# Kernel optimization log

Measured on AMD Instinct MI355X. Metric: run time of the kernel, lower is better.

The kernel has to match this reference:

```python
import jax, jax.numpy as jnp
import numpy as np

ALPHA = 0.5
GAMMA = 0.001
BIG = 1e10  # stand-in for +inf on DP borders (DILATE uses 1e10 in dtw_grad)

B, L, DIM = 32, 512, 16


def softdtw_single(D, gamma):
    """Soft-DTW value for one [N,N] cost matrix via anti-diagonal wavefront.
    Padded grid Rp[(N+1),(N+1)]: Rp[0,0]=0, borders=BIG,
    Rp[i,j] = D[i-1,j-1] + softmin_gamma(Rp[i-1,j], Rp[i-1,j-1], Rp[i,j-1]).
    Returns Rp[N,N]."""
    N = D.shape[0]
    ii = jnp.arange(N + 1)
    diag0 = jnp.full((N + 1,), BIG, D.dtype).at[0].set(0.0)  # diagonal d=0
    diag1 = jnp.full((N + 1,), BIG, D.dtype)                 # diagonal d=1 (borders)

    def step(carry, d):
        prev2, prev1 = carry  # diagonals d-2, d-1; prev1[i] = Rp[i, d-1-i]
        j = d - ii
        valid = (ii >= 1) & (ii <= N) & (j >= 1) & (j <= N)
        dval = D[jnp.clip(ii - 1, 0, N - 1), jnp.clip(j - 1, 0, N - 1)]
        a = jnp.roll(prev1, 1).at[0].set(BIG)  # Rp[i-1, j]
        b = jnp.roll(prev2, 1).at[0].set(BIG)  # Rp[i-1, j-1]
        c = prev1                               # Rp[i, j-1]
        sm = -gamma * jax.nn.logsumexp(jnp.stack([a, b, c]) * (-1.0 / gamma), axis=0)
        cur = jnp.where(valid, dval + sm, BIG)
        return (prev1, cur), None

    (_, last), _ = jax.lax.scan(step, (diag0, diag1), jnp.arange(2, 2 * N + 1))
    return last[N]


def batched_sq_dists(x, y):
    # dist[b,i,j] = clamp(||x[b,i]-y[b,j]||^2, 0)
    xn = jnp.sum(x * x, -1)[:, :, None]
    yn = jnp.sum(y * y, -1)[:, None, :]
    return jnp.clip(xn + yn - 2.0 * jnp.einsum('bid,bjd->bij', x, y), 0.0)


def dilate_loss(inp, tgt):
    # base=None path: shift input so its first step is at the origin
    x = inp - inp[:, 0:1, :]
    D = batched_sq_dists(tgt, x)  # D[b] = pairwise_distances(target[b], input[b])
    # SoftDTW value and soft alignment path (= grad of value wrt D, as in DILATE PathDTW)
    vals, paths = jax.vmap(jax.value_and_grad(lambda Dk: softdtw_single(Dk, GAMMA)))(D)
    loss_shape = jnp.mean(vals)
    N = D.shape[1]
    idx = jnp.arange(N, dtype=D.dtype)
    Omega = (idx[:, None] - idx[None, :]) ** 2  # pairwise sq dists of arange(N)
    path = jnp.mean(paths, axis=0)
    loss_temporal = jnp.sum(path * Omega) / (N * N)
    return ALPHA * loss_shape + (1.0 - ALPHA) * loss_temporal


def setup_inputs() -> dict:
    key = jax.random.key(0)
    k1, k2 = jax.random.split(key)
    inp = jax.random.normal(k1, (B, L, DIM), dtype=jnp.float32)
    tgt = jax.random.normal(k2, (B, L, DIM), dtype=jnp.float32)
    return {"input": inp, "target": tgt}


def reference(input, target):
    return dilate_loss(input, target)
```

## Files before the change

kernel.cpp:

```cpp
#include <hip/hip_runtime.h>
#include <stdint.h>


#define N 512
#define NB 32
#define BIGF 1e10f

typedef unsigned int u32;
typedef float f32x4 __attribute__((ext_vector_type(4)));

__global__ __launch_bounds__(512) void kA(const float* __restrict__ inp,
                                          const float* __restrict__ tgt,
                                          float* __restrict__ Dg) {
    const int b = blockIdx.y;
    const int jc = blockIdx.x;
    const int tid = (int)threadIdx.x;
    __shared__ float xs[4][16];
    if (tid < 64) {
        int c = tid >> 4, d = tid & 15;
        int j = jc * 4 + c;
        xs[c][d] = inp[(((size_t)b * N + j) << 4) + d] -
                   inp[(((size_t)b * N) << 4) + d];
    }
    __syncthreads();
    const float4* t4 = (const float4*)(tgt + (((size_t)b * N + tid) << 4));
    float4 ta = t4[0], tb = t4[1], tc = t4[2], td = t4[3];
    float* out = Dg + ((size_t)b * N + (size_t)jc * 4) * N + tid;
#pragma unroll
    for (int c = 0; c < 4; ++c) {
        float s = 0.f, e;
        e = ta.x - xs[c][0];  s = fmaf(e, e, s);
        e = ta.y - xs[c][1];  s = fmaf(e, e, s);
        e = ta.z - xs[c][2];  s = fmaf(e, e, s);
        e = ta.w - xs[c][3];  s = fmaf(e, e, s);
        e = tb.x - xs[c][4];  s = fmaf(e, e, s);
        e = tb.y - xs[c][5];  s = fmaf(e, e, s);
        e = tb.z - xs[c][6];  s = fmaf(e, e, s);
        e = tb.w - xs[c][7];  s = fmaf(e, e, s);
        e = tc.x - xs[c][8];  s = fmaf(e, e, s);
        e = tc.y - xs[c][9];  s = fmaf(e, e, s);
        e = tc.z - xs[c][10]; s = fmaf(e, e, s);
        e = tc.w - xs[c][11]; s = fmaf(e, e, s);
        e = td.x - xs[c][12]; s = fmaf(e, e, s);
        e = td.y - xs[c][13]; s = fmaf(e, e, s);
        e = td.z - xs[c][14]; s = fmaf(e, e, s);
        e = td.w - xs[c][15]; s = fmaf(e, e, s);
        out[(size_t)c * N] = s;
    }
}

__global__ __launch_bounds__(64) void kFT(const float* __restrict__ Dg,
                                          float* __restrict__ acc) {
    const int b = blockIdx.x;
    const int l = (int)threadIdx.x;
    const float* Db = Dg + (size_t)b * N * N;

    f32x4 A0[4], A1[4], B0[4], B1[4];
    const float* pS[4];

#define LOADC(s_, Tt)                                                         \
    do {                                                                      \
        int c_ = min(max(2 * ((Tt) - l), 0), 510);                            \
        const float* p_ = Db + ((size_t)c_ << 9) + (l << 3);                  \
        A0[s_] = ((const f32x4*)p_)[0];  A1[s_] = ((const f32x4*)p_)[1];      \
        B0[s_] = ((const f32x4*)(p_ + 512))[0];                               \
        B1[s_] = ((const f32x4*)(p_ + 512))[1];                               \
    } while (0)

#define LOADP(s_)                                                             \
    do {                                                                      \
        A0[s_] = ((const f32x4*)pS[s_])[0];                                   \
        A1[s_] = ((const f32x4*)pS[s_])[1];                                   \
        B0[s_] = ((const f32x4*)(pS[s_] + 512))[0];                           \
        B1[s_] = ((const f32x4*)(pS[s_] + 512))[1];                           \
        pS[s_] += 4096;                                                       \
    } while (0)

    float Rprev[8], Tprev[8];
#pragma unroll
    for (int r = 0; r < 8; ++r) { Rprev[r] = BIGF; Tprev[r] = 0.f; }
    float sA = BIGF, sB = BIGF, sBold = BIGF;
    float tA = 0.f, tB = 0.f, tBold = 0.f;
    float Rfin = 0.f, Tfin = 0.f;
    float dbA = (float)(10 * l);

    LOADC(0, 0); LOADC(1, 1); LOADC(2, 2); LOADC(3, 3);

#define MSTEP(T_, s_, PH)                                                     \
    do {                                                                      \
        const int cpair = (T_) - l;                                           \
        const bool valid = (PH == 1) || ((unsigned)cpair < 256u);             \
        float dA0 = (l == 0) ? BIGF : sBold;                                  \
        if (PH == 0) dA0 = (l == 0 && (T_) == 0) ? 0.f : dA0;                 \
        const float upA0 = (l == 0) ? BIGF : sA;                              \
        const float upB0 = (l == 0) ? BIGF : sB;                              \
        const float dA0T = (l == 0) ? 0.f : tBold;                            \
        const float upA0T = (l == 0) ? 0.f : tA;                              \
        const float upB0T = (l == 0) ? 0.f : tB;                              \
        const float dbB = dbA - 1.0f;                                         \
        float RcA[8], RcB[8], TcA[8], TcB[8];                                 \
        _Pragma("unroll") for (int r = 0; r < 8; ++r) {                       \
            float up = (r == 0) ? upA0 : RcA[r - 1];                          \
            float dg = (r == 0) ? dA0 : Rprev[r - 1];                         \
            float lf = Rprev[r];                                              \
            float upT = (r == 0) ? upA0T : TcA[r - 1];                        \
            float dgT = (r == 0) ? dA0T : Tprev[r - 1];                       \
            float lfT = Tprev[r];                                             \
            float mn = fminf(up, fminf(dg, lf));                              \
            float Ts = (mn == dg) ? dgT : ((mn == up) ? upT : lfT);           \
            float dr = dbA + (float)r;                                        \
            TcA[r] = fmaf(dr, dr, Ts);                                        \
            RcA[r] = ((r < 4) ? A0[s_][(r) & 3] : A1[s_][(r) & 3]) + mn;      \
        }                                                                     \
        _Pragma("unroll") for (int r = 0; r < 8; ++r) {                       \
            float up = (r == 0) ? upB0 : RcB[r - 1];                          \
            float dg = (r == 0) ? upA0 : RcA[r - 1];                          \
            float lf = RcA[r];                                                \
            float upT = (r == 0) ? upB0T : TcB[r - 1];                        \
            float dgT = (r == 0) ? upA0T : TcA[r - 1];                        \
            float lfT = TcA[r];                                               \
            float mn = fminf(up, fminf(dg, lf));                              \
            float Ts = (mn == dg) ? dgT : ((mn == up) ? upT : lfT);           \
            float dr = dbB + (float)r;                                        \
            TcB[r] = fmaf(dr, dr, Ts);                                        \
            RcB[r] = ((r < 4) ? B0[s_][(r) & 3] : B1[s_][(r) & 3]) + mn;      \
        }                                                                     \
        if (PH == 1) {                                                        \
            _Pragma("unroll") for (int r = 0; r < 8; ++r) {                   \
                Rprev[r] = RcB[r]; Tprev[r] = TcB[r];                         \
            }                                                                 \
        } else {                                                              \
            _Pragma("unroll") for (int r = 0; r < 8; ++r) {                   \
                Rprev[r] = valid ? RcB[r] : Rprev[r];                         \
                Tprev[r] = valid ? TcB[r] : Tprev[r];                         \
            }                                                                 \
        }                                                                     \
        float exA = RcA[7], exB = RcB[7], exAT = TcA[7], exBT = TcB[7];       \
        if (PH != 1) {                                                        \
            exA = valid ? exA : BIGF;                                         \
            exB = valid ? exB : BIGF;                                         \
            exAT = valid ? exAT : 0.f;                                        \
            exBT = valid ? exBT : 0.f;                                        \
        }                                                                     \
        if (PH == 2) {                                                        \
            if (cpair == 255) { Rfin = RcB[7]; Tfin = TcB[7]; }               \
        }                                                                     \
        sBold = sB; tBold = tB;                                               \
        sA = __shfl_up(exA, 1);                                               \
        sB = __shfl_up(exB, 1);                                               \
        tA = __shfl_up(exAT, 1);                                              \
        tB = __shfl_up(exBT, 1);                                              \
        dbA -= 2.0f;                                                          \
        if (PH == 1) { LOADP(s_); } else { LOADC(s_, (T_) + 4); }             \
    } while (0)

    for (int T = 0; T < 64; T += 4) {
        MSTEP(T + 0, 0, 0); MSTEP(T + 1, 1, 0);
        MSTEP(T + 2, 2, 0); MSTEP(T + 3, 3, 0);
    }
#pragma unroll
    for (int s = 0; s < 4; ++s)
        pS[s] = Db + ((size_t)(2 * (68 + s - l)) << 9) + (l << 3);
    for (int T = 64; T < 252; T += 4) {
        MSTEP(T + 0, 0, 1); MSTEP(T + 1, 1, 1);
        MSTEP(T + 2, 2, 1); MSTEP(T + 3, 3, 1);
    }
    for (int T = 252; T < 320; T += 4) {
        MSTEP(T + 0, 0, 2); MSTEP(T + 1, 1, 2);
        MSTEP(T + 2, 2, 2); MSTEP(T + 3, 3, 2);
    }
#undef MSTEP
#undef LOADC
#undef LOADP

    if (l == 63) {
        acc[b] = Rfin;
        acc[NB + b] = Tfin;
    }
}

__global__ void kC(const float* __restrict__ acc, float* __restrict__ out) {
    const int l = (int)threadIdx.x;
    float vs = (l < NB) ? acc[l] : 0.f;
    float vt = (l < NB) ? acc[NB + l] : 0.f;
#pragma unroll
    for (int o = 32; o >= 1; o >>= 1) {
        vs += __shfl_down(vs, o);
        vt += __shfl_down(vt, o);
    }
    if (l == 0)
        out[0] = 0.5f * (vs / (float)NB) +
                 0.5f * (vt / ((float)NB * (float)(N * N)));
}

__global__ void kSentinel(float* out) { out[0] = -12345.0f; }

extern "C" void kernel_launch(void* const* d_in, const int* in_sizes, int n_in,
                              void* d_out, int out_size, void* d_ws, size_t ws_size,
                              hipStream_t stream) {
    const float* inp = (const float*)d_in[0];
    const float* tgt = (const float*)d_in[1];
    float* out = (float*)d_out;

    const size_t DSZ = (size_t)NB * N * N * sizeof(float);
    const size_t NEEDED = 256 + DSZ;
    if (ws_size < NEEDED) {
        kSentinel<<<1, 1, 0, stream>>>(out);
        return;
    }
    char* ws = (char*)d_ws;
    float* acc = (float*)ws;
    float* Dg = (float*)(ws + 256);

    kA<<<dim3(N / 4, NB), 512, 0, stream>>>(inp, tgt, Dg);
    kFT<<<NB, 64, 0, stream>>>(Dg, acc);
    kC<<<1, 64, 0, stream>>>(acc, out);
}
```

Measured before the change: 123.5 us.

## Process four columns per wavefront step with DPP lane shifts

The hard-min DTW wavefront kernel now has each lane handle 8 rows by 4 columns per step instead of 8x2. This cuts the wavefront step count from 320 to 192 and so fewer serial cross-lane exchanges are needed. The prefetch pipeline is reduced from 4 to 2 stages, each loading twice the data. Lane shifts use a DPP row-shift builtin instead of __shfl_up, and a sched_barrier pins instruction order at each step. The validity masking used for the early and late phases was removed. This relies on clamped loads and BIG propagation staying correct, and it raises register pressure.

Measured after the change: 132.8 us. 7.5% more time.

```diff
diff --git a/kernel.cpp b/kernel.cpp
--- a/kernel.cpp
+++ b/kernel.cpp
@@ -8,6 +8,12 @@
 
 typedef unsigned int u32;
 typedef float f32x4 __attribute__((ext_vector_type(4)));
+
+#if __has_builtin(__builtin_amdgcn_mov_dpp)
+#define SHFL1(x) __int_as_float(__builtin_amdgcn_mov_dpp(__float_as_int(x), 0x138, 0xF, 0xF, true))
+#else
+#define SHFL1(x) __shfl_up((x), 1)
+#endif
 
 __global__ __launch_bounds__(512) void kA(const float* __restrict__ inp,
                                           const float* __restrict__ tgt,
@@ -55,121 +61,92 @@
     const int l = (int)threadIdx.x;
     const float* Db = Dg + (size_t)b * N * N;
 
-    f32x4 A0[4], A1[4], B0[4], B1[4];
-    const float* pS[4];
+    f32x4 DA[2][4], DB[2][4];
+    const float* pS[2];
 
 #define LOADC(s_, Tt)                                                         \
     do {                                                                      \
-        int c_ = min(max(2 * ((Tt) - l), 0), 510);                            \
-        const float* p_ = Db + ((size_t)c_ << 9) + (l << 3);                  \
-        A0[s_] = ((const f32x4*)p_)[0];  A1[s_] = ((const f32x4*)p_)[1];      \
-        B0[s_] = ((const f32x4*)(p_ + 512))[0];                               \
-        B1[s_] = ((const f32x4*)(p_ + 512))[1];                               \
+        int c0_ = min(max(4 * ((Tt) - l), 0), 508);                           \
+        const float* p_ = Db + ((size_t)c0_ << 9) + (l << 3);                 \
+        DA[s_][0] = ((const f32x4*)p_)[0];        DB[s_][0] = ((const f32x4*)p_)[1]; \
+        DA[s_][1] = ((const f32x4*)(p_ + 512))[0];  DB[s_][1] = ((const f32x4*)(p_ + 512))[1]; \
+        DA[s_][2] = ((const f32x4*)(p_ + 1024))[0]; DB[s_][2] = ((const f32x4*)(p_ + 1024))[1]; \
+        DA[s_][3] = ((const f32x4*)(p_ + 1536))[0]; DB[s_][3] = ((const f32x4*)(p_ + 1536))[1]; \
     } while (0)
 
 #define LOADP(s_)                                                             \
     do {                                                                      \
-        A0[s_] = ((const f32x4*)pS[s_])[0];                                   \
-        A1[s_] = ((const f32x4*)pS[s_])[1];                                   \
-        B0[s_] = ((const f32x4*)(pS[s_] + 512))[0];                           \
-        B1[s_] = ((const f32x4*)(pS[s_] + 512))[1];                           \
-        pS[s_] += 4096;                                                       \
+        const float* p_ = pS[s_];                                             \
+        DA[s_][0] = ((const f32x4*)p_)[0];        DB[s_][0] = ((const f32x4*)p_)[1]; \
+        DA[s_][1] = ((const f32x4*)(p_ + 512))[0];  DB[s_][1] = ((const f32x4*)(p_ + 512))[1]; \
+        DA[s_][2] = ((const f32x4*)(p_ + 1024))[0]; DB[s_][2] = ((const f32x4*)(p_ + 1024))[1]; \
+        DA[s_][3] = ((const f32x4*)(p_ + 1536))[0]; DB[s_][3] = ((const f32x4*)(p_ + 1536))[1]; \
+        pS[s_] += 4096;                                          \
     } while (0)
 
-    float Rprev[8], Tprev[8];
+    float Rp_[8], Tp_[8];
+    float X[8], XT[8], Y[8], YT[8];
 #pragma unroll
-    for (int r = 0; r < 8; ++r) { Rprev[r] = BIGF; Tprev[r] = 0.f; }
-    float sA = BIGF, sB = BIGF, sBold = BIGF;
-    float tA = 0.f, tB = 0.f, tBold = 0.f;
+    for (int r = 0; r < 8; ++r) { Rp_[r] = BIGF; Tp_[r] = 0.f; }
+    float sR0 = BIGF, sR1 = BIGF, sR2 = BIGF, sR3 = BIGF, sRold = BIGF;
+    float tR0 = 0.f, tR1 = 0.f, tR2 = 0.f, tR3 = 0.f, tRold = 0.f;
+    float db = (float)(12 * l);
     float Rfin = 0.f, Tfin = 0.f;
-    float dbA = (float)(10 * l);
 
-    LOADC(0, 0); LOADC(1, 1); LOADC(2, 2); LOADC(3, 3);
+    LOADC(0, 0); LOADC(1, 1);
+
+#define CELLS(upB, dgB, utB, dtB, DL, DH, pr, pt, cr, ct, dbq)                \
+    _Pragma("unroll") for (int r = 0; r < 8; ++r) {                           \
+        float up = (r == 0) ? (upB) : cr[r - 1];                              \
+        float dg = (r == 0) ? (dgB) : pr[r - 1];                              \
+        float lf = pr[r];                                                     \
+        float ut = (r == 0) ? (utB) : ct[r - 1];                              \
+        float dt = (r == 0) ? (dtB) : pt[r - 1];                              \
+        float lt = pt[r];                                                     \
+        float mn = fminf(up, fminf(dg, lf));                                  \
+        float Ts = (mn == dg) ? dt : ((mn == up) ? ut : lt);                  \
+        float dr = (dbq) + (float)r;                                          \
+        ct[r] = fmaf(dr, dr, Ts);                                             \
+        cr[r] = ((r < 4) ? (DL)[r & 3] : (DH)[r & 3]) + mn;                   \
+    }
 
 #define MSTEP(T_, s_, PH)                                                     \
     do {                                                                      \
-        const int cpair = (T_) - l;                                           \
-        const bool valid = (PH == 1) || ((unsigned)cpair < 256u);             \
-        float dA0 = (l == 0) ? BIGF : sBold;                                  \
-        if (PH == 0) dA0 = (l == 0 && (T_) == 0) ? 0.f : dA0;                 \
-        const float upA0 = (l == 0) ? BIGF : sA;                              \
-        const float upB0 = (l == 0) ? BIGF : sB;                              \
-        const float dA0T = (l == 0) ? 0.f : tBold;                            \
-        const float upA0T = (l == 0) ? 0.f : tA;                              \
-        const float upB0T = (l == 0) ? 0.f : tB;                              \
-        const float dbB = dbA - 1.0f;                                         \
-        float RcA[8], RcB[8], TcA[8], TcB[8];                                 \
-        _Pragma("unroll") for (int r = 0; r < 8; ++r) {                       \
-            float up = (r == 0) ? upA0 : RcA[r - 1];                          \
-            float dg = (r == 0) ? dA0 : Rprev[r - 1];                         \
-            float lf = Rprev[r];                                              \
-            float upT = (r == 0) ? upA0T : TcA[r - 1];                        \
-            float dgT = (r == 0) ? dA0T : Tprev[r - 1];                       \
-            float lfT = Tprev[r];                                             \
-            float mn = fminf(up, fminf(dg, lf));                              \
-            float Ts = (mn == dg) ? dgT : ((mn == up) ? upT : lfT);           \
-            float dr = dbA + (float)r;                                        \
-            TcA[r] = fmaf(dr, dr, Ts);                                        \
-            RcA[r] = ((r < 4) ? A0[s_][(r) & 3] : A1[s_][(r) & 3]) + mn;      \
+        const int cg = (T_) - l;                                              \
+        const bool z = (l == 0);                                              \
+        float u0 = z ? BIGF : sR0, u1 = z ? BIGF : sR1;                       \
+        float u2 = z ? BIGF : sR2, u3 = z ? BIGF : sR3;                       \
+        float v0 = z ? 0.f : tR0, v1 = z ? 0.f : tR1;                         \
+        float v2 = z ? 0.f : tR2, v3 = z ? 0.f : tR3;                         \
+        float g0 = z ? (((PH) == 0 && (T_) == 0) ? 0.f : BIGF) : sRold;       \
+        float h0 = z ? 0.f : tRold;                                           \
+        CELLS(u0, g0, v0, h0, DA[s_][0], DB[s_][0], Rp_, Tp_, X, XT, db);     \
+        float b0 = X[7], bt0 = XT[7];                                         \
+        CELLS(u1, u0, v1, v0, DA[s_][1], DB[s_][1], X, XT, Y, YT, db - 1.f);  \
+        float b1 = Y[7], bt1 = YT[7];                                         \
+        CELLS(u2, u1, v2, v1, DA[s_][2], DB[s_][2], Y, YT, X, XT, db - 2.f);  \
+        float b2 = X[7], bt2 = XT[7];                                         \
+        CELLS(u3, u2, v3, v2, DA[s_][3], DB[s_][3], X, XT, Rp_, Tp_, db - 3.f); \
+        float b3 = Rp_[7], bt3 = Tp_[7];                                      \
+        if ((PH) == 2) {                                                      \
+            Rfin = (cg == 127) ? Rp_[7] : Rfin;                               \
+            Tfin = (cg == 127) ? Tp_[7] : Tfin;                               \
         }                                                                     \
-        _Pragma("unroll") for (int r = 0; r < 8; ++r) {                       \
-            float up = (r == 0) ? upB0 : RcB[r - 1];                          \
-            float dg = (r == 0) ? upA0 : RcA[r - 1];                          \
-            float lf = RcA[r];                                                \
-            float upT = (r == 0) ? upB0T : TcB[r - 1];                        \
-            float dgT = (r == 0) ? upA0T : TcA[r - 1];                        \
-            float lfT = TcA[r];                                               \
-            float mn = fminf(up, fminf(dg, lf));                              \
-            float Ts = (mn == dg) ? dgT : ((mn == up) ? upT : lfT);           \
-            float dr = dbB + (float)r;                                        \
-            TcB[r] = fmaf(dr, dr, Ts);                                        \
-            RcB[r] = ((r < 4) ? B0[s_][(r) & 3] : B1[s_][(r) & 3]) + mn;      \
-        }                                                                     \
-        if (PH == 1) {                                                        \
-            _Pragma("unroll") for (int r = 0; r < 8; ++r) {                   \
-                Rprev[r] = RcB[r]; Tprev[r] = TcB[r];                         \
-            }                                                                 \
-        } else {                                                              \
-            _Pragma("unroll") for (int r = 0; r < 8; ++r) {                   \
-                Rprev[r] = valid ? RcB[r] : Rprev[r];                         \
-                Tprev[r] = valid ? TcB[r] : Tprev[r];                         \
-            }                                                                 \
-        }                                                                     \
-        float exA = RcA[7], exB = RcB[7], exAT = TcA[7], exBT = TcB[7];       \
-        if (PH != 1) {                                                        \
-            exA = valid ? exA : BIGF;                                         \
-            exB = valid ? exB : BIGF;                                         \
-            exAT = valid ? exAT : 0.f;                                        \
-            exBT = valid ? exBT : 0.f;                                        \
-        }                                                                     \
-        if (PH == 2) {                                                        \
-            if (cpair == 255) { Rfin = RcB[7]; Tfin = TcB[7]; }               \
-        }                                                                     \
-        sBold = sB; tBold = tB;                                               \
-        sA = __shfl_up(exA, 1);                                               \
-        sB = __shfl_up(exB, 1);                                               \
-        tA = __shfl_up(exAT, 1);                                              \
-        tB = __shfl_up(exBT, 1);                                              \
-        dbA -= 2.0f;                                                          \
-        if (PH == 1) { LOADP(s_); } else { LOADC(s_, (T_) + 4); }             \
+        sRold = sR3; tRold = tR3;                                             \
+        sR0 = SHFL1(b0); sR1 = SHFL1(b1); sR2 = SHFL1(b2); sR3 = SHFL1(b3);   \
+        tR0 = SHFL1(bt0); tR1 = SHFL1(bt1); tR2 = SHFL1(bt2); tR3 = SHFL1(bt3); \
+        db -= 4.0f;                                                           \
+        if ((PH) == 1) { LOADP(s_); } else { LOADC(s_, (T_) + 2); }           \
+        __builtin_amdgcn_sched_barrier(0);     \
     } while (0)
 
-    for (int T = 0; T < 64; T += 4) {
-        MSTEP(T + 0, 0, 0); MSTEP(T + 1, 1, 0);
-        MSTEP(T + 2, 2, 0); MSTEP(T + 3, 3, 0);
-    }
-#pragma unroll
-    for (int s = 0; s < 4; ++s)
-        pS[s] = Db + ((size_t)(2 * (68 + s - l)) << 9) + (l << 3);
-    for (int T = 64; T < 252; T += 4) {
-        MSTEP(T + 0, 0, 1); MSTEP(T + 1, 1, 1);
-        MSTEP(T + 2, 2, 1); MSTEP(T + 3, 3, 1);
-    }
-    for (int T = 252; T < 320; T += 4) {
-        MSTEP(T + 0, 0, 2); MSTEP(T + 1, 1, 2);
-        MSTEP(T + 2, 2, 2); MSTEP(T + 3, 3, 2);
-    }
+    for (int T = 0; T < 64; T += 2) { MSTEP(T, 0, 0); MSTEP(T + 1, 1, 0); }
+    pS[0] = Db + ((size_t)(4 * (66 - l)) << 9) + (l << 3);
+    pS[1] = Db + ((size_t)(4 * (67 - l)) << 9) + (l << 3);
+    for (int T = 64; T < 124; T += 2) { MSTEP(T, 0, 1); MSTEP(T + 1, 1, 1); }
+    for (int T = 124; T < 192; T += 2) { MSTEP(T, 0, 2); MSTEP(T + 1, 1, 2); }
 #undef MSTEP
+#undef CELLS
 #undef LOADC
 #undef LOADP
 
```
